# Optimization experiments

Measured on AMD Instinct MI355X. Metric: run time of the kernel, lower is better.

The kernel has to match this reference:

```python
import jax, jax.numpy as jnp
import numpy as np

EMBED_DIM = 1024
NUM_HEADS = 16
HEAD_DIM = EMBED_DIM // NUM_HEADS
B, S = 2, 2048


def setup_inputs() -> dict:
    key = jax.random.key(0)
    ks = jax.random.split(key, 5)
    scale = 1.0 / np.sqrt(EMBED_DIM)
    return {
        "inputs": jax.random.normal(ks[0], (B, S, EMBED_DIM), dtype=jnp.float32),
        "Wq": jax.random.normal(ks[1], (EMBED_DIM, EMBED_DIM), dtype=jnp.float32) * scale,
        "bq": jnp.zeros((EMBED_DIM,), dtype=jnp.float32),
        "Wk": jax.random.normal(ks[2], (EMBED_DIM, EMBED_DIM), dtype=jnp.float32) * scale,
        "bk": jnp.zeros((EMBED_DIM,), dtype=jnp.float32),
        "Wv": jax.random.normal(ks[3], (EMBED_DIM, EMBED_DIM), dtype=jnp.float32) * scale,
        "bv": jnp.zeros((EMBED_DIM,), dtype=jnp.float32),
        "Wo": jax.random.normal(ks[4], (EMBED_DIM, EMBED_DIM), dtype=jnp.float32) * scale,
        "bo": jnp.zeros((EMBED_DIM,), dtype=jnp.float32),
    }


def _split_heads(x):
    # [B, S, E] -> [B, H, S, Dh]
    b, s, _ = x.shape
    return x.reshape(b, s, NUM_HEADS, HEAD_DIM).transpose(0, 2, 1, 3)


def reference(inputs, Wq, bq, Wk, bk, Wv, bv, Wo, bo):
    q = _split_heads(inputs @ Wq + bq)  # [B, H, S, Dh]
    k = _split_heads(inputs @ Wk + bk)
    v = _split_heads(inputs @ Wv + bv)
    scale = 1.0 / jnp.sqrt(jnp.asarray(HEAD_DIM, dtype=q.dtype))
    scores = jnp.einsum("bhqd,bhkd->bhqk", q, k) * scale  # [B, H, S, S]
    weights = jax.nn.softmax(scores, axis=-1)
    attn = jnp.einsum("bhqk,bhkd->bhqd", weights, v)  # [B, H, S, Dh]
    concat = attn.transpose(0, 2, 1, 3).reshape(inputs.shape[0], -1, EMBED_DIM)
    return concat @ Wo + bo
```

## Files before the change

kernel.cpp:

```cpp
#include <hip/hip_runtime.h>


#define QSCALE 0.18033688011112042f

using bf16x8 = __attribute__((ext_vector_type(8))) short;
using f32x16 = __attribute__((ext_vector_type(16))) float;
using u16x8  = __attribute__((ext_vector_type(8))) unsigned short;

__device__ __forceinline__ unsigned short f2bf(float f) {
  unsigned int u = __float_as_uint(f);
  u += 0x7fffu + ((u >> 16) & 1u);
  return (unsigned short)(u >> 16);
}

__device__ __forceinline__ void gload_lds16(const unsigned short* g, unsigned short* l) {
  __builtin_amdgcn_global_load_lds(
      (const __attribute__((address_space(1))) unsigned int*)g,
      (__attribute__((address_space(3))) unsigned int*)l, 16, 0, 0);
}

__global__ void conv_prep_kernel(const float* __restrict__ x, unsigned short* __restrict__ y,
                                 const float* __restrict__ W0, const float* __restrict__ W1,
                                 const float* __restrict__ W2, const float* __restrict__ W3,
                                 unsigned short* __restrict__ out) {
  __shared__ float t[32][33];
  int blk = blockIdx.x;
  if (blk >= 4096) {
    int i = (blk - 4096) * 256 + threadIdx.x;
    const float4* xf = (const float4*)x;
    float4 a = xf[i * 2], b = xf[i * 2 + 1];
    u16x8 o;
    o[0] = f2bf(a.x); o[1] = f2bf(a.y); o[2] = f2bf(a.z); o[3] = f2bf(a.w);
    o[4] = f2bf(b.x); o[5] = f2bf(b.y); o[6] = f2bf(b.z); o[7] = f2bf(b.w);
    *((u16x8*)y + i) = o;
    return;
  }
  int z = blk >> 10, rem = blk & 1023;
  const float* W = (z == 0) ? W0 : (z == 1) ? W1 : (z == 2) ? W2 : W3;
  unsigned short* o = out + (size_t)z * 1024 * 1024;
  int kt = (rem >> 5) * 32, nt = (rem & 31) * 32;
  int tx = threadIdx.x & 31, ty = threadIdx.x >> 5;
#pragma unroll
  for (int i = 0; i < 4; ++i)
    t[ty + i * 8][tx] = W[(size_t)(kt + ty + i * 8) * 1024 + nt + tx];
  __syncthreads();
#pragma unroll
  for (int i = 0; i < 4; ++i)
    o[(size_t)(nt + ty + i * 8) * 1024 + kt + tx] = f2bf(t[tx][ty + i * 8]);
}

__global__ __launch_bounds__(256) void gemm_bt_kernel(
    const unsigned short* __restrict__ A, const unsigned short* __restrict__ Bt,
    int mode, const float* __restrict__ bias0, const float* __restrict__ bias1,
    const float* __restrict__ bias2, unsigned short* __restrict__ Qh,
    unsigned short* __restrict__ Kh, unsigned short* __restrict__ Vt,
    float* __restrict__ Out) {
  const int K = 1024;
  __shared__ unsigned short SMEM[16384];

  int id = blockIdx.y * gridDim.x + blockIdx.x;
  int xcd = id & 7, pos = id >> 3;
  int bxr = pos >> 2, byr = xcd * 4 + (pos & 3);
  int n0 = bxr * 128, m0 = byr * 128;
  int tid = threadIdx.x;
  int w = tid >> 6, lane = tid & 63, l31 = lane & 31, half = lane >> 5;
  int wm = w >> 1, wn = w & 1;

  f32x16 acc[2][2];
#pragma unroll
  for (int i = 0; i < 2; ++i)
#pragma unroll
    for (int j = 0; j < 2; ++j)
#pragma unroll
      for (int r = 0; r < 16; ++r) acc[i][j][r] = 0.f;

  int srow = lane >> 2;
  int gchunk = (lane & 3) ^ ((srow >> 1) & 3);
  const unsigned short* Ag = A + (size_t)(m0 + 32 * w + srow) * K + gchunk * 8;
  const unsigned short* Bg = Bt + (size_t)(n0 + 32 * w + srow) * K + gchunk * 8;
  unsigned short* Asw = &SMEM[w * 1024];
  unsigned short* Bsw = &SMEM[8192 + w * 1024];

#pragma unroll
  for (int j = 0; j < 2; ++j) {
    gload_lds16(Ag + (size_t)(16 * j) * K, Asw + j * 512);
    gload_lds16(Bg + (size_t)(16 * j) * K, Bsw + j * 512);
  }

  for (int it = 0; it < 32; ++it) {
    int cur = (it & 1) * 4096;
    __syncthreads();
    if (it + 1 < 32) {
      int nxt = ((it + 1) & 1) * 4096;
      int kk = (it + 1) * 32;
#pragma unroll
      for (int j = 0; j < 2; ++j) {
        gload_lds16(Ag + kk + (size_t)(16 * j) * K, Asw + nxt + j * 512);
        gload_lds16(Bg + kk + (size_t)(16 * j) * K, Bsw + nxt + j * 512);
      }
    }
    const unsigned short* Asl = &SMEM[cur];
    const unsigned short* Bsl = &SMEM[8192 + cur];
#pragma unroll
    for (int kc = 0; kc < 2; ++kc) {
      int swk = (l31 >> 1) & 3;
      int ph = ((kc * 2 + half) ^ swk) * 8;
      bf16x8 af[2], bfr[2];
#pragma unroll
      for (int mt = 0; mt < 2; ++mt)
        af[mt] = *(bf16x8*)&Asl[(wm * 64 + mt * 32 + l31) * 32 + ph];
#pragma unroll
      for (int nt = 0; nt < 2; ++nt)
        bfr[nt] = *(bf16x8*)&Bsl[(wn * 64 + nt * 32 + l31) * 32 + ph];
#pragma unroll
      for (int mt = 0; mt < 2; ++mt)
#pragma unroll
        for (int nt = 0; nt < 2; ++nt)
          acc[mt][nt] = __builtin_amdgcn_mfma_f32_32x32x16_bf16(af[mt], bfr[nt], acc[mt][nt], 0, 0, 0);
    }
  }

  if (mode == 1) {
#pragma unroll
    for (int mt = 0; mt < 2; ++mt)
#pragma unroll
      for (int nt = 0; nt < 2; ++nt)
#pragma unroll
        for (int r = 0; r < 16; ++r) {
          int row = (r & 3) + 8 * (r >> 2) + 4 * half;
          int gm = m0 + wm * 64 + mt * 32 + row;
          int gn = n0 + wn * 64 + nt * 32 + l31;
          Out[(size_t)gm * 1024 + gn] = acc[mt][nt][r] + bias0[gn];
        }
    return;
  }

  int btype = bxr >> 3;
  if (btype < 2) {
    const float* bp = btype ? bias1 : bias0;
    unsigned short* dst = btype ? Kh : Qh;
    float sc = btype ? 1.0f : QSCALE;
#pragma unroll
    for (int mt = 0; mt < 2; ++mt)
#pragma unroll
      for (int nt = 0; nt < 2; ++nt)
#pragma unroll
        for (int r = 0; r < 16; ++r) {
          int row = (r & 3) + 8 * (r >> 2) + 4 * half;
          int gm = m0 + wm * 64 + mt * 32 + row;
          int gn = n0 + wn * 64 + nt * 32 + l31;
          int e = gn & 1023;
          float v = (acc[mt][nt][r] + bp[e]) * sc;
          int hh = e >> 6, d = e & 63;
          int bb = gm >> 11, s = gm & 2047;
          dst[(((size_t)(bb * 16 + hh)) * 2048 + s) * 64 + d] = f2bf(v);
        }
  } else {
    __syncthreads();
    unsigned short* T = SMEM;
#pragma unroll
    for (int mt = 0; mt < 2; ++mt)
#pragma unroll
      for (int nt = 0; nt < 2; ++nt)
#pragma unroll
        for (int r = 0; r < 16; ++r) {
          int row = (r & 3) + 8 * (r >> 2) + 4 * half;
          int sl = wm * 64 + mt * 32 + row;
          int dl = wn * 64 + nt * 32 + l31;
          int e = (n0 - 2048) + dl;
          float v = acc[mt][nt][r] + bias2[e];
          T[dl * 128 + (sl ^ ((dl & 15) << 3))] = f2bf(v);
        }
    __syncthreads();
    int bb = m0 >> 11, s0 = m0 & 2047;
    int h0 = (n0 - 2048) >> 6;
    int rr0 = tid >> 2, csub = tid & 3;
#pragma unroll
    for (int pass = 0; pass < 2; ++pass) {
      int rr = rr0 + 64 * pass;
      int hh = h0 + (rr >> 6), d = rr & 63;
      unsigned short* vrow = Vt + (((size_t)(bb * 16 + hh)) * 64 + d) * 2048 + s0;
#pragma unroll
      for (int c = 0; c < 4; ++c) {
        int cc = c * 4 + csub;
        uint4 val = *(uint4*)&T[rr * 128 + ((cc ^ (rr & 15)) * 8)];
        *(uint4*)&vrow[cc * 8] = val;
      }
    }
  }
}

__global__ __launch_bounds__(256, 2) void attn_kernel(
    const unsigned short* __restrict__ Qh, const unsigned short* __restrict__ Kh,
    const unsigned short* __restrict__ Vt, unsigned short* __restrict__ Ctx) {
  __shared__ __align__(16) unsigned short SM[32768];

  int bx = blockIdx.x;
  int xcd = bx & 7, tt = bx >> 3;
  int qt = tt & 15;
  int bhi = (tt >> 4) * 8 + xcd;
  int h = bhi & 15, b = bhi >> 4;

  int tid = threadIdx.x;
  int w = tid >> 6, lane = tid & 63, l31 = lane & 31, half = lane >> 5;
  int l7 = l31 & 7;
  int mw = w & 1, kw = w >> 1;

  size_t bh = (size_t)bhi;
  const unsigned short* Qb  = Qh + (bh * 2048 + (size_t)qt * 128) * 64;
  const unsigned short* Kbh = Kh + bh * 131072;
  const unsigned short* Vbh = Vt + bh * 131072;

  bf16x8 qf0[4], qf1[4];
#pragma unroll
  for (int kc = 0; kc < 4; ++kc) {
    qf0[kc] = *(const bf16x8*)&Qb[(size_t)(mw * 64 + l31) * 64 + kc * 16 + half * 8];
    qf1[kc] = *(const bf16x8*)&Qb[(size_t)(mw * 64 + 32 + l31) * 64 + kc * 16 + half * 8];
  }

  int r8 = lane >> 3, gc = (lane & 7) ^ r8;
  const unsigned short* gbase;
  int gstep; size_t segstep;
  if (w < 2) { gbase = Kbh + (size_t)(w * 1024 + r8) * 64 + gc * 8; gstep = 4096; segstep = 512; }
  else       { gbase = Vbh + (size_t)r8 * 2048 + (w - 2) * 1024 + gc * 8; gstep = 64; segstep = 16384; }
  unsigned short* lb = SM + w * 4096;

#pragma unroll
  for (int j = 0; j < 8; ++j) gload_lds16(gbase + j * segstep, lb + j * 512);
  gbase += gstep;

  f32x16 o00, o01, o10, o11;
#pragma unroll
  for (int r = 0; r < 16; ++r) { o00[r] = 0.f; o01[r] = 0.f; o10[r] = 0.f; o11[r] = 0.f; }
  float l0 = 0.f, l1 = 0.f;

  for (int i = 0; i < 16; ++i) {
    __syncthreads();
    if (i < 15) {
      unsigned short* nb = lb + (((i + 1) & 1) << 14);
#pragma unroll
      for (int j = 0; j < 8; ++j) gload_lds16(gbase + j * segstep, nb + j * 512);
      gbase += gstep;
    }
    const unsigned short* cur = SM + ((i & 1) << 14);
    const unsigned short* Ksw = cur + kw * 4096;
    const unsigned short* Vsw = cur + 8192 + kw * 4096;

    f32x16 s00, s01, s10, s11;
#pragma unroll
    for (int r = 0; r < 16; ++r) { s00[r] = 0.f; s01[r] = 0.f; s10[r] = 0.f; s11[r] = 0.f; }
    __builtin_amdgcn_s_setprio(1);
#pragma unroll
    for (int kc = 0; kc < 4; ++kc) {
      int ph = ((kc * 2 + half) ^ l7) * 8;
      bf16x8 kb0 = *(bf16x8*)&Ksw[l31 * 64 + ph];
      bf16x8 kb1 = *(bf16x8*)&Ksw[(32 + l31) * 64 + ph];
      s00 = __builtin_amdgcn_mfma_f32_32x32x16_bf16(kb0, qf0[kc], s00, 0, 0, 0);
      s01 = __builtin_amdgcn_mfma_f32_32x32x16_bf16(kb1, qf0[kc], s01, 0, 0, 0);
      s10 = __builtin_amdgcn_mfma_f32_32x32x16_bf16(kb0, qf1[kc], s10, 0, 0, 0);
      s11 = __builtin_amdgcn_mfma_f32_32x32x16_bf16(kb1, qf1[kc], s11, 0, 0, 0);
    }
    __builtin_amdgcn_s_setprio(0);

    bf16x8 U0[4], U1[4];
    auto smx = [&](const f32x16& sa, const f32x16& sb, float& lacc, bf16x8* U) {
      float pa[16], pb[16];
#pragma unroll
      for (int r = 0; r < 16; ++r) {
        pa[r] = __builtin_amdgcn_exp2f(sa[r]);
        pb[r] = __builtin_amdgcn_exp2f(sb[r]);
      }
      float t0 = 0.f, t1 = 0.f, t2 = 0.f, t3 = 0.f;
#pragma unroll
      for (int r = 0; r < 16; r += 4) {
        t0 += pa[r] + pb[r]; t1 += pa[r + 1] + pb[r + 1];
        t2 += pa[r + 2] + pb[r + 2]; t3 += pa[r + 3] + pb[r + 3];
      }
      lacc += (t0 + t1) + (t2 + t3);
      unsigned int own[16];
#pragma unroll
      for (int m = 0; m < 4; ++m)
#pragma unroll
        for (int p = 0; p < 2; ++p) {
          int r = 4 * m + 2 * p;
          unsigned int wa, wb;
          asm("v_cvt_pk_bf16_f32 %0, %1, %2" : "=v"(wa) : "v"(pa[r]), "v"(pa[r + 1]));
          asm("v_cvt_pk_bf16_f32 %0, %1, %2" : "=v"(wb) : "v"(pb[r]), "v"(pb[r + 1]));
          own[2 * m + p] = wa;
          own[2 * m + 8 + p] = wb;
        }
#pragma unroll
      for (int kc = 0; kc < 4; ++kc) {
        unsigned int a0 = own[4 * kc],     b0 = own[4 * kc + 2];
        unsigned int a1 = own[4 * kc + 1], b1 = own[4 * kc + 3];
        asm("v_permlane32_swap_b32 %0, %1" : "+v"(a0), "+v"(b0));
        asm("v_permlane32_swap_b32 %0, %1" : "+v"(a1), "+v"(b1));
        union { unsigned int u[4]; bf16x8 v; } Uu;
        Uu.u[0] = a0; Uu.u[1] = a1; Uu.u[2] = b0; Uu.u[3] = b1;
        U[kc] = Uu.v;
      }
    };
    smx(s00, s01, l0, U0);
    smx(s10, s11, l1, U1);

    __builtin_amdgcn_s_setprio(1);
#pragma unroll
    for (int kc = 0; kc < 4; ++kc) {
      int ph = ((kc * 2 + half) ^ l7) * 8;
      bf16x8 vb0 = *(bf16x8*)&Vsw[l31 * 64 + ph];
      bf16x8 vb1 = *(bf16x8*)&Vsw[(32 + l31) * 64 + ph];
      o00 = __builtin_amdgcn_mfma_f32_32x32x16_bf16(U0[kc], vb0, o00, 0, 0, 0);
      o01 = __builtin_amdgcn_mfma_f32_32x32x16_bf16(U0[kc], vb1, o01, 0, 0, 0);
      o10 = __builtin_amdgcn_mfma_f32_32x32x16_bf16(U1[kc], vb0, o10, 0, 0, 0);
      o11 = __builtin_amdgcn_mfma_f32_32x32x16_bf16(U1[kc], vb1, o11, 0, 0, 0);
    }
    __builtin_amdgcn_s_setprio(0);
  }

  float lw0 = l0 + __shfl_xor(l0, 32);
  float lw1 = l1 + __shfl_xor(l1, 32);
  __syncthreads();
  float* mrgO = (float*)SM;
  float* mrgL = (float*)SM + 8192;
  if (kw == 1) {
    auto dump = [&](const f32x16& a0, const f32x16& a1, float lw, int qg) {
      float* dst = mrgO + (mw * 2 + qg) * 2048 + lane * 32;
#pragma unroll
      for (int c = 0; c < 8; ++c) {
        float4 t;
        if (c < 4) t = make_float4(a0[4 * c], a0[4 * c + 1], a0[4 * c + 2], a0[4 * c + 3]);
        else       t = make_float4(a1[4 * (c - 4)], a1[4 * (c - 4) + 1], a1[4 * (c - 4) + 2], a1[4 * (c - 4) + 3]);
        *(float4*)&dst[(c ^ l7) * 4] = t;
      }
      if (half == 0) mrgL[(mw * 2 + qg) * 32 + l31] = lw;
    };
    dump(o00, o01, lw0, 0);
    dump(o10, o11, lw1, 1);
  }
  __syncthreads();
  if (kw == 0) {
    auto fin = [&](f32x16& a0, f32x16& a1, float lw, int qg) {
      const float* src = mrgO + (mw * 2 + qg) * 2048 + lane * 32;
#pragma unroll
      for (int c = 0; c < 8; ++c) {
        float4 t = *(const float4*)&src[(c ^ l7) * 4];
        if (c < 4) { a0[4 * c] += t.x; a0[4 * c + 1] += t.y; a0[4 * c + 2] += t.z; a0[4 * c + 3] += t.w; }
        else       { a1[4 * (c - 4)] += t.x; a1[4 * (c - 4) + 1] += t.y; a1[4 * (c - 4) + 2] += t.z; a1[4 * (c - 4) + 3] += t.w; }
      }
      lw += mrgL[(mw * 2 + qg) * 32 + l31];
      float inv = 1.0f / lw;
#pragma unroll
      for (int r = 0; r < 16; ++r) {
        int rmap = (r & 3) + 8 * (r >> 2) + 4 * half;
        float invr = __shfl(inv, rmap);
        size_t row = (size_t)(b * 2048 + qt * 128 + mw * 64 + qg * 32 + rmap);
        Ctx[row * 1024 + h * 64 + l31]      = f2bf(a0[r] * invr);
        Ctx[row * 1024 + h * 64 + 32 + l31] = f2bf(a1[r] * invr);
      }
    };
    fin(o00, o01, lw0, 0);
    fin(o10, o11, lw1, 1);
  }
}

extern "C" void kernel_launch(void* const* d_in, const int* in_sizes, int n_in,
                              void* d_out, int out_size, void* d_ws, size_t ws_size,
                              hipStream_t stream) {
  const float* X  = (const float*)d_in[0];
  const float* Wq = (const float*)d_in[1];
  const float* bq = (const float*)d_in[2];
  const float* Wk = (const float*)d_in[3];
  const float* bk = (const float*)d_in[4];
  const float* Wv = (const float*)d_in[5];
  const float* bv = (const float*)d_in[6];
  const float* Wo = (const float*)d_in[7];
  const float* bo = (const float*)d_in[8];

  if (ws_size < (size_t)48 * 1024 * 1024) return;

  char* ws = (char*)d_ws;
  unsigned short* Xbf = (unsigned short*)(ws);
  unsigned short* Wt  = (unsigned short*)(ws + ((size_t)8 << 20));
  unsigned short* Qh  = (unsigned short*)(ws + ((size_t)16 << 20));
  unsigned short* Kh  = (unsigned short*)(ws + ((size_t)24 << 20));
  unsigned short* Vt  = (unsigned short*)(ws + ((size_t)32 << 20));
  unsigned short* Ctx = (unsigned short*)(ws + ((size_t)40 << 20));
  unsigned short* WtO = Wt + (size_t)3 * 1024 * 1024;

  conv_prep_kernel<<<6144, 256, 0, stream>>>(X, Xbf, Wq, Wk, Wv, Wo, Wt);
  gemm_bt_kernel<<<dim3(24, 32), 256, 0, stream>>>(Xbf, Wt, 0, bq, bk, bv, Qh, Kh, Vt, nullptr);
  attn_kernel<<<dim3(512), 256, 0, stream>>>(Qh, Kh, Vt, Ctx);
  gemm_bt_kernel<<<dim3(8, 32), 256, 0, stream>>>(Ctx, WtO, 1, bo, bo, bo, nullptr, nullptr, nullptr, (float*)d_out);
}
```

Measured before the change: 188.6 us.

## Double attention query tile to 256 rows with 512-thread blocks sharing K/V tiles

The attention kernel now runs 8 waves per block covering 256 query rows instead of 4 waves covering 128, halving the grid. Each K/V tile staged in shared memory is reused by twice as many query rows, and each wave issues half as many async loads. The final cross-wave merge runs in two phases so it fits the existing shared buffer. Risks include fewer blocks (256 across the CUs), lower occupancy under the 512-thread launch bound, and extra barriers in the epilogue.

```diff
diff --git a/kernel.cpp b/kernel.cpp
--- a/kernel.cpp
+++ b/kernel.cpp
@@ -190,24 +190,24 @@
   }
 }
 
-__global__ __launch_bounds__(256, 2) void attn_kernel(
+__global__ __launch_bounds__(512, 2) void attn_kernel(
     const unsigned short* __restrict__ Qh, const unsigned short* __restrict__ Kh,
     const unsigned short* __restrict__ Vt, unsigned short* __restrict__ Ctx) {
   __shared__ __align__(16) unsigned short SM[32768];
 
   int bx = blockIdx.x;
   int xcd = bx & 7, tt = bx >> 3;
-  int qt = tt & 15;
-  int bhi = (tt >> 4) * 8 + xcd;
+  int qt = tt & 7;
+  int bhi = (tt >> 3) * 8 + xcd;
   int h = bhi & 15, b = bhi >> 4;
 
   int tid = threadIdx.x;
   int w = tid >> 6, lane = tid & 63, l31 = lane & 31, half = lane >> 5;
   int l7 = l31 & 7;
-  int mw = w & 1, kw = w >> 1;
+  int mw = w & 3, kw = w >> 2;
 
   size_t bh = (size_t)bhi;
-  const unsigned short* Qb  = Qh + (bh * 2048 + (size_t)qt * 128) * 64;
+  const unsigned short* Qb  = Qh + (bh * 2048 + (size_t)qt * 256) * 64;
   const unsigned short* Kbh = Kh + bh * 131072;
   const unsigned short* Vbh = Vt + bh * 131072;
 
@@ -219,15 +219,21 @@
   }
 
   int r8 = lane >> 3, gc = (lane & 7) ^ r8;
-  const unsigned short* gbase;
-  int gstep; size_t segstep;
-  if (w < 2) { gbase = Kbh + (size_t)(w * 1024 + r8) * 64 + gc * 8; gstep = 4096; segstep = 512; }
-  else       { gbase = Vbh + (size_t)r8 * 2048 + (w - 2) * 1024 + gc * 8; gstep = 64; segstep = 16384; }
-  unsigned short* lb = SM + w * 4096;
-
-#pragma unroll
-  for (int j = 0; j < 8; ++j) gload_lds16(gbase + j * segstep, lb + j * 512);
-  gbase += gstep;
+  int t = w >> 1, s0 = (w & 1) * 4;
+  const unsigned short* gb[4];
+  int lofs[4];
+  int gstep;
+#pragma unroll
+  for (int j = 0; j < 4; ++j) {
+    int s = s0 + j;
+    if (t < 2) { gb[j] = Kbh + (size_t)(t * 1024 + s * 8 + r8) * 64 + gc * 8; }
+    else       { gb[j] = Vbh + (size_t)(s * 8 + r8) * 2048 + (t - 2) * 1024 + gc * 8; }
+    lofs[j] = t * 4096 + s * 512;
+  }
+  gstep = (t < 2) ? 4096 : 64;
+
+#pragma unroll
+  for (int j = 0; j < 4; ++j) { gload_lds16(gb[j], SM + lofs[j]); gb[j] += gstep; }
 
   f32x16 o00, o01, o10, o11;
 #pragma unroll
@@ -237,10 +243,9 @@
   for (int i = 0; i < 16; ++i) {
     __syncthreads();
     if (i < 15) {
-      unsigned short* nb = lb + (((i + 1) & 1) << 14);
-#pragma unroll
-      for (int j = 0; j < 8; ++j) gload_lds16(gbase + j * segstep, nb + j * 512);
-      gbase += gstep;
+      unsigned short* nb = SM + (((i + 1) & 1) << 14);
+#pragma unroll
+      for (int j = 0; j < 4; ++j) { gload_lds16(gb[j], nb + lofs[j]); gb[j] += gstep; }
     }
     const unsigned short* cur = SM + ((i & 1) << 14);
     const unsigned short* Ksw = cur + kw * 4096;
@@ -322,44 +327,50 @@
   __syncthreads();
   float* mrgO = (float*)SM;
   float* mrgL = (float*)SM + 8192;
-  if (kw == 1) {
-    auto dump = [&](const f32x16& a0, const f32x16& a1, float lw, int qg) {
-      float* dst = mrgO + (mw * 2 + qg) * 2048 + lane * 32;
-#pragma unroll
-      for (int c = 0; c < 8; ++c) {
-        float4 t;
-        if (c < 4) t = make_float4(a0[4 * c], a0[4 * c + 1], a0[4 * c + 2], a0[4 * c + 3]);
-        else       t = make_float4(a1[4 * (c - 4)], a1[4 * (c - 4) + 1], a1[4 * (c - 4) + 2], a1[4 * (c - 4) + 3]);
-        *(float4*)&dst[(c ^ l7) * 4] = t;
-      }
-      if (half == 0) mrgL[(mw * 2 + qg) * 32 + l31] = lw;
-    };
-    dump(o00, o01, lw0, 0);
-    dump(o10, o11, lw1, 1);
-  }
-  __syncthreads();
-  if (kw == 0) {
-    auto fin = [&](f32x16& a0, f32x16& a1, float lw, int qg) {
-      const float* src = mrgO + (mw * 2 + qg) * 2048 + lane * 32;
-#pragma unroll
-      for (int c = 0; c < 8; ++c) {
-        float4 t = *(const float4*)&src[(c ^ l7) * 4];
-        if (c < 4) { a0[4 * c] += t.x; a0[4 * c + 1] += t.y; a0[4 * c + 2] += t.z; a0[4 * c + 3] += t.w; }
-        else       { a1[4 * (c - 4)] += t.x; a1[4 * (c - 4) + 1] += t.y; a1[4 * (c - 4) + 2] += t.z; a1[4 * (c - 4) + 3] += t.w; }
-      }
-      lw += mrgL[(mw * 2 + qg) * 32 + l31];
-      float inv = 1.0f / lw;
-#pragma unroll
-      for (int r = 0; r < 16; ++r) {
-        int rmap = (r & 3) + 8 * (r >> 2) + 4 * half;
-        float invr = __shfl(inv, rmap);
-        size_t row = (size_t)(b * 2048 + qt * 128 + mw * 64 + qg * 32 + rmap);
-        Ctx[row * 1024 + h * 64 + l31]      = f2bf(a0[r] * invr);
-        Ctx[row * 1024 + h * 64 + 32 + l31] = f2bf(a1[r] * invr);
-      }
-    };
-    fin(o00, o01, lw0, 0);
-    fin(o10, o11, lw1, 1);
+  int slot2 = (mw & 1) * 2;
+  int phase = mw >> 1;
+#pragma unroll
+  for (int p = 0; p < 2; ++p) {
+    if (kw == 1 && phase == p) {
+      auto dump = [&](const f32x16& a0, const f32x16& a1, float lw, int qg) {
+        float* dst = mrgO + (slot2 + qg) * 2048 + lane * 32;
+#pragma unroll
+        for (int c = 0; c < 8; ++c) {
+          float4 t4;
+          if (c < 4) t4 = make_float4(a0[4 * c], a0[4 * c + 1], a0[4 * c + 2], a0[4 * c + 3]);
+          else       t4 = make_float4(a1[4 * (c - 4)], a1[4 * (c - 4) + 1], a1[4 * (c - 4) + 2], a1[4 * (c - 4) + 3]);
+          *(float4*)&dst[(c ^ l7) * 4] = t4;
+        }
+        if (half == 0) mrgL[(slot2 + qg) * 32 + l31] = lw;
+      };
+      dump(o00, o01, lw0, 0);
+      dump(o10, o11, lw1, 1);
+    }
+    __syncthreads();
+    if (kw == 0 && phase == p) {
+      auto fin = [&](f32x16& a0, f32x16& a1, float lw, int qg) {
+        const float* src = mrgO + (slot2 + qg) * 2048 + lane * 32;
+#pragma unroll
+        for (int c = 0; c < 8; ++c) {
+          float4 t4 = *(const float4*)&src[(c ^ l7) * 4];
+          if (c < 4) { a0[4 * c] += t4.x; a0[4 * c + 1] += t4.y; a0[4 * c + 2] += t4.z; a0[4 * c + 3] += t4.w; }
+          else       { a1[4 * (c - 4)] += t4.x; a1[4 * (c - 4) + 1] += t4.y; a1[4 * (c - 4) + 2] += t4.z; a1[4 * (c - 4) + 3] += t4.w; }
+        }
+        lw += mrgL[(slot2 + qg) * 32 + l31];
+        float inv = 1.0f / lw;
+#pragma unroll
+        for (int r = 0; r < 16; ++r) {
+          int rmap = (r & 3) + 8 * (r >> 2) + 4 * half;
+          float invr = __shfl(inv, rmap);
+          size_t row = (size_t)(b * 2048 + qt * 256 + mw * 64 + qg * 32 + rmap);
+          Ctx[row * 1024 + h * 64 + l31]      = f2bf(a0[r] * invr);
+          Ctx[row * 1024 + h * 64 + 32 + l31] = f2bf(a1[r] * invr);
+        }
+      };
+      fin(o00, o01, lw0, 0);
+      fin(o10, o11, lw1, 1);
+    }
+    __syncthreads();
   }
 }
 
@@ -389,6 +400,6 @@
 
   conv_prep_kernel<<<6144, 256, 0, stream>>>(X, Xbf, Wq, Wk, Wv, Wo, Wt);
   gemm_bt_kernel<<<dim3(24, 32), 256, 0, stream>>>(Xbf, Wt, 0, bq, bk, bv, Qh, Kh, Vt, nullptr);
-  attn_kernel<<<dim3(512), 256, 0, stream>>>(Qh, Kh, Vt, Ctx);
+  attn_kernel<<<dim3(256), 512, 0, stream>>>(Qh, Kh, Vt, Ctx);
   gemm_bt_kernel<<<dim3(8, 32), 256, 0, stream>>>(Ctx, WtO, 1, bo, bo, bo, nullptr, nullptr, nullptr, (float*)d_out);
 }
```

Measured after the change: 183.0 us (median of 2 runs). 3.0% less time.
